# Performance work log

Measured on AMD Instinct MI355X. Metric: run time of the kernel, lower is better.

## Reference

```python
import jax, jax.numpy as jnp
import numpy as np

MARGIN = 0.2  # init margin


def setup_inputs() -> dict:
    key = jax.random.key(0)
    k1, k2, k3, k4 = jax.random.split(key, 4)
    B, Li_raw, Ls_raw, D = 128, 65, 67, 1024
    im_set = jax.random.normal(k1, (B, Li_raw, D), dtype=jnp.float32)
    s_seq = jax.random.normal(k2, (B, Ls_raw, D), dtype=jnp.float32)
    # raw lengths; forward uses im_len-1 and s_len-3, keep them well in range
    im_len = jax.random.randint(k3, (B,), 10, Li_raw + 1)
    s_len = jax.random.randint(k4, (B,), 10, Ls_raw + 1)
    return {"im_set": im_set, "s_seq": s_seq, "im_len": im_len, "s_len": s_len}


def reference(im_set, s_seq, im_len, s_len):
    # slice off CLS-like tokens, as in the torch module
    im = im_set[:, 1:, :]        # [Bi, Li, D]
    s = s_seq[:, 1:-2, :]        # [Bs, Ls, D]
    im_l = im_len - 1
    s_l = s_len - 3
    Bi, Li, D = im.shape
    Bs, Ls, _ = s.shape

    # 4D alignment: all image-batch x sentence-batch token-pair dot products
    align = jnp.einsum('bid,tjd->btij', im, s)  # [Bi, Bs, Li, Ls]

    # length masks (True = padded position), matching the torch loops
    im_mask = jnp.arange(Li)[None, :] >= im_l[:, None]  # [Bi, Li]
    s_mask = jnp.arange(Ls)[None, :] >= s_l[:, None]    # [Bs, Ls]
    mask = im_mask[:, None, :, None] | s_mask[None, :, None, :]
    align = jnp.where(mask, 0.0, align)

    # aggregation 'MrSw': max over image regions, sum over words
    aggr = align.max(axis=2).sum(axis=2)  # [Bi, Bs]

    # contrastive hinge loss with max violation
    diag = jnp.diag(aggr)[:, None]  # [B, 1]
    eye = jnp.eye(Bi, dtype=bool)
    cost_s = jnp.where(eye, 0.0, jnp.maximum(MARGIN + aggr - diag, 0.0))
    cost_im = jnp.where(eye, 0.0, jnp.maximum(MARGIN + aggr - diag.T, 0.0))
    loss = cost_s.max(axis=1).sum() + cost_im.max(axis=0).sum()
    return loss
```

## Files before the change

### kernel.cpp

```cpp
#include <hip/hip_runtime.h>

typedef __attribute__((ext_vector_type(4))) int   i32x4;
typedef __attribute__((ext_vector_type(8))) int   i32x8;
typedef __attribute__((ext_vector_type(16))) float f32x16;

__device__ __forceinline__ unsigned enc4(float v) {
    unsigned s = (__float_as_uint(v) >> 31) << 3;
    float a = fabsf(v);
    unsigned c = a < 0.25f ? 0u : a < 0.75f ? 1u : a < 1.25f ? 2u : a < 1.75f ? 3u
               : a < 2.5f  ? 4u : a < 3.5f  ? 5u : a < 5.0f  ? 6u : 7u;
    return s | c;
}

__global__ void conv_kernel(const float* __restrict__ im, const int* __restrict__ iml,
                            const float* __restrict__ ss, const int* __restrict__ sl,
                            unsigned* __restrict__ Ad, unsigned* __restrict__ Bd)
{
    int bid = blockIdx.x;
    const float* src; const int* len; unsigned* dst; int rawL, adj;
    if (bid < 4096) { src = im; len = iml; dst = Ad; rawL = 65; adj = -1; }
    else { bid -= 4096; src = ss; len = sl; dst = Bd; rawL = 67; adj = -3; }
    int t = threadIdx.x;
    int m = bid * 2 + (t >> 7);
    int c = (t & 127) * 8;
    int b = m >> 6;
    int i = m & 63;
    int lim = len[b] + adj;
    float4 v0 = make_float4(0.f, 0.f, 0.f, 0.f), v1 = v0;
    if (i < lim) {
        const float* p = src + ((size_t)(b * rawL + 1 + i) << 10) + c;
        v0 = *(const float4*)p;
        v1 = *(const float4*)(p + 4);
    }
    unsigned w = enc4(v0.x) | (enc4(v0.y) << 4) | (enc4(v0.z) << 8)  | (enc4(v0.w) << 12)
               | (enc4(v1.x) << 16) | (enc4(v1.y) << 20) | (enc4(v1.z) << 24) | (enc4(v1.w) << 28);
    dst[(m >> 8) * 32768 + (c >> 6) * 2048 + ((c >> 5) & 1) * 1024
        + (m & 255) * 4 + ((c >> 3) & 3)] = w;
}

__device__ __forceinline__ void gload_lds16(const void* g, void* l) {
    __builtin_amdgcn_global_load_lds((const __attribute__((address_space(1))) void*)g,
                                     (__attribute__((address_space(3))) void*)l,
                                     16, 0, 0);
}

__device__ __forceinline__ i32x8 dup4(i32x4 a) {
    return __builtin_shufflevector(a, a, 0, 1, 2, 3, 0, 1, 2, 3);
}

__global__ void __launch_bounds__(512) gemm_aggr_kernel(const unsigned char* __restrict__ A,
                                                        const unsigned char* __restrict__ B,
                                                        float* __restrict__ aggr)
{
    __shared__ __align__(16) char As[3][16384];
    __shared__ __align__(16) char Bs[3][16384];

    const int tid  = threadIdx.x;
    const int lane = tid & 63;
    const int wid  = tid >> 6;
    const int wr   = wid >> 2;
    const int wc   = wid & 3;
    const int tm   = blockIdx.y;
    const int tn   = blockIdx.x;

    const int r31 = lane & 31;
    const int g2  = lane >> 5;

    const unsigned char* gA_t = A + (size_t)tm * 131072 + tid * 16;
    const unsigned char* gB_t = B + (size_t)tn * 131072 + tid * 16;

#define STAGE(j)                                                              \
    gload_lds16(gA_t + (2*(j))   * 8192, As[(j) % 3]        + tid * 16);      \
    gload_lds16(gA_t + (2*(j)+1) * 8192, As[(j) % 3] + 8192 + tid * 16);      \
    gload_lds16(gB_t + (2*(j))   * 8192, Bs[(j) % 3]        + tid * 16);      \
    gload_lds16(gB_t + (2*(j)+1) * 8192, Bs[(j) % 3] + 8192 + tid * 16);

    f32x16 acc[4][2];
#pragma unroll
    for (int mi = 0; mi < 4; ++mi)
#pragma unroll
        for (int ni = 0; ni < 2; ++ni)
#pragma unroll
            for (int r = 0; r < 16; ++r)
                acc[mi][ni][r] = 0.f;

    const int aOff = g2 * 4096 + (wr * 128 + r31) * 16;
    const int bOff = g2 * 4096 + (wc * 64 + r31) * 16;

    i32x4 faE[4], fbE[2], faO[4], fbO[2];

#define READF(FA, FB, Ab, Bb)                                               \
    FA[0] = *(const i32x4*)((Ab) + aOff);                                   \
    FA[1] = *(const i32x4*)((Ab) + aOff + 512);                             \
    FA[2] = *(const i32x4*)((Ab) + aOff + 1024);                            \
    FA[3] = *(const i32x4*)((Ab) + aOff + 1536);                            \
    FB[0] = *(const i32x4*)((Bb) + bOff);                                   \
    FB[1] = *(const i32x4*)((Bb) + bOff + 512);

    STAGE(0)
    STAGE(1)
    asm volatile("s_waitcnt vmcnt(4)" ::: "memory");
    __builtin_amdgcn_s_barrier();
    __builtin_amdgcn_sched_barrier(0);
    READF(faE, fbE, As[0], Bs[0])

#define MFMA8(CA, CB)                                                       \
    __builtin_amdgcn_s_setprio(1);                                          \
    acc[0][0] = __builtin_amdgcn_mfma_scale_f32_32x32x64_f8f6f4(            \
        dup4(CA[0]), dup4(CB[0]), acc[0][0], 4, 4, 0, 127, 0, 127);         \
    acc[0][1] = __builtin_amdgcn_mfma_scale_f32_32x32x64_f8f6f4(            \
        dup4(CA[0]), dup4(CB[1]), acc[0][1], 4, 4, 0, 127, 0, 127);         \
    acc[1][0] = __builtin_amdgcn_mfma_scale_f32_32x32x64_f8f6f4(            \
        dup4(CA[1]), dup4(CB[0]), acc[1][0], 4, 4, 0, 127, 0, 127);         \
    acc[1][1] = __builtin_amdgcn_mfma_scale_f32_32x32x64_f8f6f4(            \
        dup4(CA[1]), dup4(CB[1]), acc[1][1], 4, 4, 0, 127, 0, 127);         \
    acc[2][0] = __builtin_amdgcn_mfma_scale_f32_32x32x64_f8f6f4(            \
        dup4(CA[2]), dup4(CB[0]), acc[2][0], 4, 4, 0, 127, 0, 127);         \
    acc[2][1] = __builtin_amdgcn_mfma_scale_f32_32x32x64_f8f6f4(            \
        dup4(CA[2]), dup4(CB[1]), acc[2][1], 4, 4, 0, 127, 0, 127);         \
    acc[3][0] = __builtin_amdgcn_mfma_scale_f32_32x32x64_f8f6f4(            \
        dup4(CA[3]), dup4(CB[0]), acc[3][0], 4, 4, 0, 127, 0, 127);         \
    acc[3][1] = __builtin_amdgcn_mfma_scale_f32_32x32x64_f8f6f4(            \
        dup4(CA[3]), dup4(CB[1]), acc[3][1], 4, 4, 0, 127, 0, 127);         \
    __builtin_amdgcn_s_setprio(0);

#define BODY(J)                                                             \
  {                                                                         \
    asm volatile("s_waitcnt vmcnt(0)" ::: "memory");                        \
    __builtin_amdgcn_s_barrier();                                           \
    __builtin_amdgcn_sched_barrier(0);                                      \
    if ((J) + 2 <= 7) { STAGE((J) + 2) }                                    \
    READF(faO, fbO, As[(J) % 3] + 8192, Bs[(J) % 3] + 8192)    \
    MFMA8(faE, fbE)                                            \
    if ((J) < 7) {                                                          \
        READF(faE, fbE, As[((J) + 1) % 3], Bs[((J) + 1) % 3])     \
    }                                                                       \
    MFMA8(faO, fbO)                                            \
  }

    BODY(0) BODY(1) BODY(2) BODY(3) BODY(4) BODY(5) BODY(6) BODY(7)
#undef STAGE
#undef READF
#undef MFMA8
#undef BODY

#pragma unroll
    for (int h = 0; h < 2; ++h) {
        float cm[2];
#pragma unroll
        for (int ni = 0; ni < 2; ++ni) {
            float m = acc[h * 2][ni][0];
#pragma unroll
            for (int dm = 0; dm < 2; ++dm)
#pragma unroll
                for (int r = 0; r < 16; ++r)
                    m = fmaxf(m, acc[h * 2 + dm][ni][r]);
            m = fmaxf(m, __shfl_xor(m, 32));
            cm[ni] = m;
        }
        float s = cm[0] + cm[1];
        s += __shfl_xor(s, 1);
        s += __shfl_xor(s, 2);
        s += __shfl_xor(s, 4);
        s += __shfl_xor(s, 8);
        s += __shfl_xor(s, 16);
        if (lane == 0) {
            int b = tm * 4 + wr * 2 + h;
            int t = tn * 4 + wc;
            aggr[b * 128 + t] = s;
        }
    }
}

__global__ void loss_stage1(const float* __restrict__ aggr, float* __restrict__ red)
{
    const int x = blockIdx.x;
    const int y = threadIdx.x;
    const float diag = aggr[x * 129];
    float ms = 0.f, mi = 0.f;
    if (y != x) {
        ms = fmaxf(0.2f + aggr[x * 128 + y] - diag, 0.f);
        mi = fmaxf(0.2f + aggr[y * 128 + x] - diag, 0.f);
    }
#pragma unroll
    for (int o = 32; o; o >>= 1) {
        ms = fmaxf(ms, __shfl_xor(ms, o));
        mi = fmaxf(mi, __shfl_xor(mi, o));
    }
    __shared__ float sm[2], si[2];
    if ((y & 63) == 0) { sm[y >> 6] = ms; si[y >> 6] = mi; }
    __syncthreads();
    if (y == 0) red[x] = fmaxf(sm[0], sm[1]) + fmaxf(si[0], si[1]);
}

__global__ void loss_stage2(const float* __restrict__ red, float* __restrict__ out)
{
    float v = red[threadIdx.x];
#pragma unroll
    for (int o = 32; o; o >>= 1) v += __shfl_xor(v, o);
    __shared__ float s[2];
    if ((threadIdx.x & 63) == 0) s[threadIdx.x >> 6] = v;
    __syncthreads();
    if (threadIdx.x == 0) *out = s[0] + s[1];
}

extern "C" void kernel_launch(void* const* d_in, const int* in_sizes, int n_in,
                              void* d_out, int out_size, void* d_ws, size_t ws_size,
                              hipStream_t stream)
{
    const float* im_set = (const float*)d_in[0];
    const float* s_seq  = (const float*)d_in[1];
    const int*   im_len = (const int*)d_in[2];
    const int*   s_len  = (const int*)d_in[3];
    float* out = (float*)d_out;

    unsigned char* Abf = (unsigned char*)d_ws;
    unsigned char* Bbf = (unsigned char*)d_ws + (4u << 20);
    float*         agg = (float*)((char*)d_ws + (8u << 20));
    float*         red = (float*)((char*)d_ws + (8u << 20) + 65536);

    conv_kernel<<<8192, 256, 0, stream>>>(im_set, im_len, s_seq, s_len,
                                          (unsigned*)Abf, (unsigned*)Bbf);

    gemm_aggr_kernel<<<dim3(32, 32), 512, 0, stream>>>(Abf, Bbf, agg);

    loss_stage1<<<128, 128, 0, stream>>>(agg, red);
    loss_stage2<<<1, 128, 0, stream>>>(red, out);
}
```

Before: 53.04 us.

## Switch GEMM K-loop to double-buffered 32KB stages with four iterations

Replaces the triple-buffered pipeline (eight K-steps of 16KB per operand, prefetch two ahead) with a double-buffered one (four K-steps of 32KB per operand, prefetch one ahead). The aim is fewer barriers and vmcnt waits per tile and more MFMA work between synchronisation points. In exchange, LDS rises from 96KB to 128KB per block and the first stage's load is fully exposed before any compute. The vmcnt(0) wait at each step also removes overlap of the next prefetch with the current compute barrier.

New measurement: 52.99 us. No clear change (-0.1%).

```diff
diff --git a/kernel.cpp b/kernel.cpp
--- a/kernel.cpp
+++ b/kernel.cpp
@@ -52,8 +52,8 @@
                                                         const unsigned char* __restrict__ B,
                                                         float* __restrict__ aggr)
 {
-    __shared__ __align__(16) char As[3][16384];
-    __shared__ __align__(16) char Bs[3][16384];
+    __shared__ __align__(16) char As[2][32768];
+    __shared__ __align__(16) char Bs[2][32768];
 
     const int tid  = threadIdx.x;
     const int lane = tid & 63;
@@ -70,10 +70,14 @@
     const unsigned char* gB_t = B + (size_t)tn * 131072 + tid * 16;
 
 #define STAGE(j)                                                              \
-    gload_lds16(gA_t + (2*(j))   * 8192, As[(j) % 3]        + tid * 16);      \
-    gload_lds16(gA_t + (2*(j)+1) * 8192, As[(j) % 3] + 8192 + tid * 16);      \
-    gload_lds16(gB_t + (2*(j))   * 8192, Bs[(j) % 3]        + tid * 16);      \
-    gload_lds16(gB_t + (2*(j)+1) * 8192, Bs[(j) % 3] + 8192 + tid * 16);
+    gload_lds16(gA_t + (4*(j))   * 8192, As[(j) & 1]         + tid * 16);     \
+    gload_lds16(gA_t + (4*(j)+1) * 8192, As[(j) & 1] +  8192 + tid * 16);     \
+    gload_lds16(gA_t + (4*(j)+2) * 8192, As[(j) & 1] + 16384 + tid * 16);     \
+    gload_lds16(gA_t + (4*(j)+3) * 8192, As[(j) & 1] + 24576 + tid * 16);     \
+    gload_lds16(gB_t + (4*(j))   * 8192, Bs[(j) & 1]         + tid * 16);     \
+    gload_lds16(gB_t + (4*(j)+1) * 8192, Bs[(j) & 1] +  8192 + tid * 16);     \
+    gload_lds16(gB_t + (4*(j)+2) * 8192, Bs[(j) & 1] + 16384 + tid * 16);     \
+    gload_lds16(gB_t + (4*(j)+3) * 8192, Bs[(j) & 1] + 24576 + tid * 16);
 
     f32x16 acc[4][2];
 #pragma unroll
@@ -96,13 +100,6 @@
     FA[3] = *(const i32x4*)((Ab) + aOff + 1536);                            \
     FB[0] = *(const i32x4*)((Bb) + bOff);                                   \
     FB[1] = *(const i32x4*)((Bb) + bOff + 512);
-
-    STAGE(0)
-    STAGE(1)
-    asm volatile("s_waitcnt vmcnt(4)" ::: "memory");
-    __builtin_amdgcn_s_barrier();
-    __builtin_amdgcn_sched_barrier(0);
-    READF(faE, fbE, As[0], Bs[0])
 
 #define MFMA8(CA, CB)                                                       \
     __builtin_amdgcn_s_setprio(1);                                          \
@@ -126,19 +123,24 @@
 
 #define BODY(J)                                                             \
   {                                                                         \
+    const char* Ab = As[(J) & 1];                                           \
+    const char* Bb = Bs[(J) & 1];                                           \
     asm volatile("s_waitcnt vmcnt(0)" ::: "memory");                        \
     __builtin_amdgcn_s_barrier();                                           \
     __builtin_amdgcn_sched_barrier(0);                                      \
-    if ((J) + 2 <= 7) { STAGE((J) + 2) }                                    \
-    READF(faO, fbO, As[(J) % 3] + 8192, Bs[(J) % 3] + 8192)    \
-    MFMA8(faE, fbE)                                            \
-    if ((J) < 7) {                                                          \
-        READF(faE, fbE, As[((J) + 1) % 3], Bs[((J) + 1) % 3])     \
-    }                                                                       \
-    MFMA8(faO, fbO)                                            \
+    if ((J) < 3) { STAGE((J) + 1) }                                         \
+    READF(faE, fbE, Ab,          Bb)                        \
+    READF(faO, fbO, Ab +  8192,  Bb +  8192)                \
+    MFMA8(faE, fbE)                                                         \
+    READF(faE, fbE, Ab + 16384,  Bb + 16384)                \
+    MFMA8(faO, fbO)                                                         \
+    READF(faO, fbO, Ab + 24576,  Bb + 24576)                \
+    MFMA8(faE, fbE)                                                         \
+    MFMA8(faO, fbO)                                                         \
   }
 
-    BODY(0) BODY(1) BODY(2) BODY(3) BODY(4) BODY(5) BODY(6) BODY(7)
+    STAGE(0)
+    BODY(0) BODY(1) BODY(2) BODY(3)
 #undef STAGE
 #undef READF
 #undef MFMA8
```
